# Kernel optimization log

Measured on AMD Instinct MI355X. Metric: run time of the kernel, lower is better.

The kernel has to match this reference:

```python
import jax, jax.numpy as jnp
import numpy as np

N, E, D, H, C, L = 50000, 600000, 128, 128, 40, 2
NEG_SLOPE = 0.1


def setup_inputs() -> dict:
    key = jax.random.key(0)
    ks = jax.random.split(key, 12)

    def lin(k, din, dout):
        return (jax.random.normal(k, (din, dout), jnp.float32) / np.sqrt(din)).astype(jnp.float32)

    x = jax.random.normal(ks[0], (N, D), jnp.float32)
    edge_index = jax.random.randint(ks[1], (2, E), 0, N, dtype=jnp.int32)
    return {
        "x": x,
        "edge_index": edge_index,
        "enc_Wl": lin(ks[2], D, H),
        "enc_Wr": lin(ks[3], D, H),
        "enc_b": jnp.zeros((H,), jnp.float32),
        "lay_Wl": jnp.stack([lin(jax.random.fold_in(ks[4], i), H, H) for i in range(L)]),
        "lay_Wr": jnp.stack([lin(jax.random.fold_in(ks[5], i), H, H) for i in range(L)]),
        "lay_b": jnp.zeros((L, H), jnp.float32),
        "dec_Wl": lin(ks[6], H, C),
        "dec_Wr": lin(ks[7], H, C),
        "dec_b": jnp.zeros((C,), jnp.float32),
    }


def _sage(x, src, dst, inv_cnt, Wl, Wr, b):
    # mean-aggregate neighbor messages: gather x[src], scatter-sum to dst, divide by degree
    agg = jax.ops.segment_sum(x[src], dst, num_segments=N) * inv_cnt  # [N, d_in]
    return agg @ Wl + x @ Wr + b


def reference(x, edge_index, enc_Wl, enc_Wr, enc_b, lay_Wl, lay_Wr, lay_b, dec_Wl, dec_Wr, dec_b):
    src, dst = edge_index[0], edge_index[1]
    # in-degree per target node, clamped to 1 (PyG scatter-mean semantics: isolated nodes get 0)
    deg = jax.ops.segment_sum(jnp.ones((E,), jnp.float32), dst, num_segments=N)
    inv_cnt = (1.0 / jnp.maximum(deg, 1.0))[:, None]  # [N, 1]

    h = jax.nn.leaky_relu(_sage(x, src, dst, inv_cnt, enc_Wl, enc_Wr, enc_b), NEG_SLOPE)
    for i in range(L):
        h = jax.nn.leaky_relu(_sage(h, src, dst, inv_cnt, lay_Wl[i], lay_Wr[i], lay_b[i]), NEG_SLOPE)
    out = _sage(h, src, dst, inv_cnt, dec_Wl, dec_Wr, dec_b)
    return jax.nn.log_softmax(out, axis=1)
```

## Files before the change

kernel.cpp:

```cpp
#include <hip/hip_runtime.h>
#include <hip/hip_bf16.h>

#define NN 50000
#define EE 600000
#define HH 128
#define CC 40
#define NEG 0.1f
#define SCAN_NB 196

typedef __attribute__((ext_vector_type(8))) short bf16x8;
typedef __attribute__((ext_vector_type(4))) float f32x4;

__device__ __forceinline__ unsigned short f2bf(float f) {
    unsigned u = __float_as_uint(f);
    unsigned r = u + 0x7fffu + ((u >> 16) & 1u);
    return (unsigned short)(r >> 16);
}
__device__ __forceinline__ float bfhi(unsigned v) { return __uint_as_float(v & 0xFFFF0000u); }
__device__ __forceinline__ float bflo(unsigned v) { return __uint_as_float(v << 16); }


__global__ void k_count(const int* __restrict__ dst, int* __restrict__ counts) {
    int t = blockIdx.x * blockDim.x + threadIdx.x;
    if (t < EE / 4) {
        int4 d = ((const int4*)dst)[t];
        if ((unsigned)d.x < (unsigned)NN) atomicAdd(&counts[d.x], 1);
        if ((unsigned)d.y < (unsigned)NN) atomicAdd(&counts[d.y], 1);
        if ((unsigned)d.z < (unsigned)NN) atomicAdd(&counts[d.z], 1);
        if ((unsigned)d.w < (unsigned)NN) atomicAdd(&counts[d.w], 1);
    }
}

__global__ void k_scanA(const int* __restrict__ counts, int* __restrict__ blocksums) {
    int t = threadIdx.x, b = blockIdx.x;
    int i = b * 256 + t;
    int v = (i < NN) ? counts[i] : 0;
    for (int off = 1; off < 64; off <<= 1) v += __shfl_xor(v, off, 64);
    __shared__ int ws[4];
    if ((t & 63) == 0) ws[t >> 6] = v;
    __syncthreads();
    if (t == 0) blocksums[b] = ws[0] + ws[1] + ws[2] + ws[3];
}

__global__ void k_scanC(const int* __restrict__ counts, const int* __restrict__ blocksums,
                        int* __restrict__ offsets, int* __restrict__ cursor,
                        float* __restrict__ inv) {
    int t = threadIdx.x, b = blockIdx.x, lane = t & 63, w = t >> 6;
    __shared__ int ws1[4];
    __shared__ int ws2[4];
    int r = (t < SCAN_NB && t < b) ? blocksums[t] : 0;
    for (int off = 1; off < 64; off <<= 1) r += __shfl_xor(r, off, 64);
    if (lane == 0) ws1[w] = r;
    __syncthreads();
    int blockoff = ws1[0] + ws1[1] + ws1[2] + ws1[3];
    int i = b * 256 + t;
    int c = (i < NN) ? counts[i] : 0;
    int v = c;
    for (int off = 1; off < 64; off <<= 1) {
        int u = __shfl_up(v, off, 64);
        if (lane >= off) v += u;
    }
    if (lane == 63) ws2[w] = v;
    __syncthreads();
    int woff = 0;
    for (int j = 0; j < w; ++j) woff += ws2[j];
    int excl = blockoff + woff + (v - c);
    if (i < NN) {
        offsets[i] = excl;
        cursor[i]  = excl;
        inv[i] = (c > 0) ? 1.0f / (float)c : 1.0f;
    }
    if (b == SCAN_NB - 1 && t == 0) offsets[NN] = blockoff + blocksums[SCAN_NB - 1];
}

__global__ void k_scatter(const int* __restrict__ src, const int* __restrict__ dst,
                          int* __restrict__ cursor, int* __restrict__ csr) {
    int t = blockIdx.x * blockDim.x + threadIdx.x;
    if (t < EE / 4) {
        int4 s = ((const int4*)src)[t];
        int4 d = ((const int4*)dst)[t];
        if ((unsigned)d.x < (unsigned)NN) csr[atomicAdd(&cursor[d.x], 1)] = s.x;
        if ((unsigned)d.y < (unsigned)NN) csr[atomicAdd(&cursor[d.y], 1)] = s.y;
        if ((unsigned)d.z < (unsigned)NN) csr[atomicAdd(&cursor[d.z], 1)] = s.z;
        if ((unsigned)d.w < (unsigned)NN) csr[atomicAdd(&cursor[d.w], 1)] = s.w;
    }
}

struct SwzArgs {
    const float* src[8];
    unsigned short* dst[8];
};

template <int DOUT, int DOUTP>
__device__ __forceinline__ void swz_one(const float* __restrict__ W,
                                        unsigned short* __restrict__ dstf, int idx) {
    int k = idx / DOUTP, n = idx % DOUTP;
    unsigned short val = (n < DOUT) ? f2bf(W[k * DOUT + n]) : (unsigned short)0;
    int kt = k >> 5, kin = k & 31, nt = n >> 4, nin = n & 15;
    int lane = ((kin >> 3) << 4) | nin;
    int j = kin & 7;
    int NT = DOUTP >> 4;
    dstf[(((kt * NT + nt) * 64) + lane) * 8 + j] = val;
}

__global__ void k_swz_all(SwzArgs a) {
    int b = blockIdx.x;
    if (b < 384) {
        int which = b >> 6;
        int idx = (b & 63) * 256 + threadIdx.x;
        swz_one<HH, HH>(a.src[which], a.dst[which], idx);
    } else {
        int bb = b - 384;
        int which = 6 + bb / 24;
        int idx = (bb % 24) * 256 + threadIdx.x;
        swz_one<CC, 48>(a.src[which], a.dst[which], idx);
    }
}

template <int NT, int MODE, int INF32>
__global__ __launch_bounds__(256) void k_fused(
    const void* __restrict__ hin_v,
    const int* __restrict__ offsets, const int* __restrict__ csr,
    const float* __restrict__ inv,
    const unsigned short* __restrict__ B1f, const unsigned short* __restrict__ B2f,
    const float* __restrict__ bias, void* __restrict__ out_v) {
    __shared__ unsigned lds[16][72];
    int wid = threadIdx.x >> 6;
    int lane = threadIdx.x & 63;
    int m0 = blockIdx.x * 16;

#pragma unroll
    for (int r = 0; r < 4; ++r) {
        int node = m0 + wid * 4 + r;
        int beg = offsets[node], end = offsets[node + 1];
        float a0 = 0.f, a1 = 0.f;
        int e = beg;
        if (INF32) {
            const float* hf = (const float*)hin_v;
            for (; e + 3 < end; e += 4) {
                int s0 = csr[e], s1 = csr[e + 1], s2 = csr[e + 2], s3 = csr[e + 3];
                float2 v0 = *(const float2*)(hf + s0 * HH + 2 * lane);
                float2 v1 = *(const float2*)(hf + s1 * HH + 2 * lane);
                float2 v2 = *(const float2*)(hf + s2 * HH + 2 * lane);
                float2 v3 = *(const float2*)(hf + s3 * HH + 2 * lane);
                a0 += (v0.x + v1.x) + (v2.x + v3.x);
                a1 += (v0.y + v1.y) + (v2.y + v3.y);
            }
            for (; e < end; ++e) {
                float2 v = *(const float2*)(hf + csr[e] * HH + 2 * lane);
                a0 += v.x; a1 += v.y;
            }
        } else {
            const unsigned* hw = (const unsigned*)hin_v;
            for (; e + 3 < end; e += 4) {
                int s0 = csr[e], s1 = csr[e + 1], s2 = csr[e + 2], s3 = csr[e + 3];
                unsigned v0 = hw[s0 * 64 + lane];
                unsigned v1 = hw[s1 * 64 + lane];
                unsigned v2 = hw[s2 * 64 + lane];
                unsigned v3 = hw[s3 * 64 + lane];
                a0 += (bflo(v0) + bflo(v1)) + (bflo(v2) + bflo(v3));
                a1 += (bfhi(v0) + bfhi(v1)) + (bfhi(v2) + bfhi(v3));
            }
            for (; e < end; ++e) {
                unsigned v = hw[csr[e] * 64 + lane];
                a0 += bflo(v); a1 += bfhi(v);
            }
        }
        float sc = inv[node];
        lds[wid * 4 + r][lane] = ((unsigned)f2bf(a1 * sc) << 16) | (unsigned)f2bf(a0 * sc);
    }
    __syncthreads();

    if (MODE == 1 && wid != 0) return;

    int nin = lane & 15;
    int kq = lane >> 4;
    const unsigned* arow = &lds[nin][0];
    constexpr int TW = (MODE == 0) ? 2 : NT;

    f32x4 acc[TW];
#pragma unroll
    for (int j = 0; j < TW; ++j) acc[j] = (f32x4){0.f, 0.f, 0.f, 0.f};

#pragma unroll
    for (int kt = 0; kt < 4; ++kt) {
        bf16x8 a1 = *(const bf16x8*)(arow + kt * 16 + kq * 4);
        bf16x8 a2;
        if (INF32) {
            const float* hf = (const float*)hin_v;
            const float* rp = hf + (m0 + nin) * HH + kt * 32 + kq * 8;
            float4 p0 = *(const float4*)(rp);
            float4 p1 = *(const float4*)(rp + 4);
            a2[0] = (short)f2bf(p0.x); a2[1] = (short)f2bf(p0.y);
            a2[2] = (short)f2bf(p0.z); a2[3] = (short)f2bf(p0.w);
            a2[4] = (short)f2bf(p1.x); a2[5] = (short)f2bf(p1.y);
            a2[6] = (short)f2bf(p1.z); a2[7] = (short)f2bf(p1.w);
        } else {
            const unsigned short* hb = (const unsigned short*)hin_v;
            a2 = *(const bf16x8*)(hb + (m0 + nin) * HH + kt * 32 + kq * 8);
        }
#pragma unroll
        for (int j = 0; j < TW; ++j) {
            int tile = (MODE == 0) ? (wid * 2 + j) : j;
            bf16x8 b1 = *(const bf16x8*)(B1f + (((kt * NT + tile) * 64) + lane) * 8);
            acc[j] = __builtin_amdgcn_mfma_f32_16x16x32_bf16(a1, b1, acc[j], 0, 0, 0);
        }
#pragma unroll
        for (int j = 0; j < TW; ++j) {
            int tile = (MODE == 0) ? (wid * 2 + j) : j;
            bf16x8 b2 = *(const bf16x8*)(B2f + (((kt * NT + tile) * 64) + lane) * 8);
            acc[j] = __builtin_amdgcn_mfma_f32_16x16x32_bf16(a2, b2, acc[j], 0, 0, 0);
        }
    }

    if (MODE == 0) {
        unsigned short* out = (unsigned short*)out_v;
#pragma unroll
        for (int j = 0; j < TW; ++j) {
            int col = (wid * 2 + j) * 16 + nin;
            float bv = bias[col];
#pragma unroll
            for (int r = 0; r < 4; ++r) {
                int m = m0 + kq * 4 + r;
                float v = acc[j][r] + bv;
                v = fmaxf(v, NEG * v);
                out[m * HH + col] = f2bf(v);
            }
        }
    } else {
        float* out = (float*)out_v;
        float bv[NT];
#pragma unroll
        for (int t = 0; t < NT; ++t) {
            int col = t * 16 + nin;
            bv[t] = (col < CC) ? bias[col] : 0.f;
        }
#pragma unroll
        for (int r = 0; r < 4; ++r) {
            int m = m0 + kq * 4 + r;
            float v[NT];
            float mx = -1e30f;
#pragma unroll
            for (int t = 0; t < NT; ++t) {
                int col = t * 16 + nin;
                v[t] = acc[t][r] + bv[t];
                if (col < CC) mx = fmaxf(mx, v[t]);
            }
            for (int off = 1; off < 16; off <<= 1) mx = fmaxf(mx, __shfl_xor(mx, off, 64));
            float sm = 0.f;
#pragma unroll
            for (int t = 0; t < NT; ++t) {
                int col = t * 16 + nin;
                if (col < CC) sm += expf(v[t] - mx);
            }
            for (int off = 1; off < 16; off <<= 1) sm += __shfl_xor(sm, off, 64);
            float lse = mx + logf(sm);
#pragma unroll
            for (int t = 0; t < NT; ++t) {
                int col = t * 16 + nin;
                if (col < CC) out[m * CC + col] = v[t] - lse;
            }
        }
    }
}

extern "C" void kernel_launch(void* const* d_in, const int* in_sizes, int n_in,
                              void* d_out, int out_size, void* d_ws, size_t ws_size,
                              hipStream_t stream) {
    const float* x      = (const float*)d_in[0];
    const int*   ei     = (const int*)d_in[1];
    const float* enc_Wl = (const float*)d_in[2];
    const float* enc_Wr = (const float*)d_in[3];
    const float* enc_b  = (const float*)d_in[4];
    const float* lay_Wl = (const float*)d_in[5];
    const float* lay_Wr = (const float*)d_in[6];
    const float* lay_b  = (const float*)d_in[7];
    const float* dec_Wl = (const float*)d_in[8];
    const float* dec_Wr = (const float*)d_in[9];
    const float* dec_b  = (const float*)d_in[10];
    float* out = (float*)d_out;

    const int* src = ei;
    const int* dst = ei + EE;

    char* p = (char*)d_ws;
    auto carve = [&](size_t bytes) {
        char* r = p;
        p += (bytes + 255) & ~(size_t)255;
        return r;
    };
    int*            counts    = (int*)carve(NN * 4);
    int*            offsets   = (int*)carve((NN + 1) * 4);
    int*            cursor    = (int*)carve(NN * 4);
    int*            csr       = (int*)carve(EE * 4);
    float*          inv       = (float*)carve(NN * 4);
    int*            blocksums = (int*)carve(SCAN_NB * 4);
    unsigned short* h1        = (unsigned short*)carve((size_t)NN * HH * 2);
    unsigned short* h2        = (unsigned short*)carve((size_t)NN * HH * 2);
    unsigned short* wf[8];
    for (int i = 0; i < 6; ++i) wf[i] = (unsigned short*)carve(HH * HH * 2);
    wf[6] = (unsigned short*)carve(HH * 48 * 2);
    wf[7] = (unsigned short*)carve(HH * 48 * 2);

    {
        SwzArgs a;
        a.src[0] = enc_Wl; a.src[1] = enc_Wr;
        a.src[2] = lay_Wl; a.src[3] = lay_Wr;
        a.src[4] = lay_Wl + HH * HH; a.src[5] = lay_Wr + HH * HH;
        a.src[6] = dec_Wl; a.src[7] = dec_Wr;
        for (int i = 0; i < 8; ++i) a.dst[i] = wf[i];
        k_swz_all<<<432, 256, 0, stream>>>(a);
    }

    hipMemsetAsync(counts, 0, NN * 4, stream);
    int eblk4 = (EE / 4 + 255) / 256;
    k_count<<<eblk4, 256, 0, stream>>>(dst, counts);
    k_scanA<<<SCAN_NB, 256, 0, stream>>>(counts, blocksums);
    k_scanC<<<SCAN_NB, 256, 0, stream>>>(counts, blocksums, offsets, cursor, inv);
    k_scatter<<<eblk4, 256, 0, stream>>>(src, dst, cursor, csr);

    const int FB = NN / 16;
    k_fused<8, 0, 1><<<FB, 256, 0, stream>>>(x,  offsets, csr, inv, wf[0], wf[1], enc_b,      h1);
    k_fused<8, 0, 0><<<FB, 256, 0, stream>>>(h1, offsets, csr, inv, wf[2], wf[3], lay_b,      h2);
    k_fused<8, 0, 0><<<FB, 256, 0, stream>>>(h2, offsets, csr, inv, wf[4], wf[5], lay_b + HH, h1);
    k_fused<3, 1, 0><<<FB, 256, 0, stream>>>(h1, offsets, csr, inv, wf[6], wf[7], dec_b,      out);
}
```

Measured before the change: 348.3 us.

## Gather multiple neighbor rows per wave with wide loads and software prefetch

Reworks the neighbor aggregation so each wave handles its four nodes at once. Lanes are split into groups that each load a full feature row with 16-byte vector loads, so several edges are in flight per wave per round. The next round's loads are issued before the current round is accumulated, and partial sums are then combined across lane groups with cross-lane shuffles. The aim is more memory-level parallelism on the latency-bound gather, at the cost of higher register use, shuffle reductions, and wasted lanes when degrees are uneven.

```diff
diff --git a/kernel.cpp b/kernel.cpp
--- a/kernel.cpp
+++ b/kernel.cpp
@@ -129,45 +129,134 @@
     int lane = threadIdx.x & 63;
     int m0 = blockIdx.x * 16;
 
-#pragma unroll
-    for (int r = 0; r < 4; ++r) {
-        int node = m0 + wid * 4 + r;
-        int beg = offsets[node], end = offsets[node + 1];
-        float a0 = 0.f, a1 = 0.f;
-        int e = beg;
-        if (INF32) {
-            const float* hf = (const float*)hin_v;
-            for (; e + 3 < end; e += 4) {
-                int s0 = csr[e], s1 = csr[e + 1], s2 = csr[e + 2], s3 = csr[e + 3];
-                float2 v0 = *(const float2*)(hf + s0 * HH + 2 * lane);
-                float2 v1 = *(const float2*)(hf + s1 * HH + 2 * lane);
-                float2 v2 = *(const float2*)(hf + s2 * HH + 2 * lane);
-                float2 v3 = *(const float2*)(hf + s3 * HH + 2 * lane);
-                a0 += (v0.x + v1.x) + (v2.x + v3.x);
-                a1 += (v0.y + v1.y) + (v2.y + v3.y);
-            }
-            for (; e < end; ++e) {
-                float2 v = *(const float2*)(hf + csr[e] * HH + 2 * lane);
-                a0 += v.x; a1 += v.y;
-            }
-        } else {
-            const unsigned* hw = (const unsigned*)hin_v;
-            for (; e + 3 < end; e += 4) {
-                int s0 = csr[e], s1 = csr[e + 1], s2 = csr[e + 2], s3 = csr[e + 3];
-                unsigned v0 = hw[s0 * 64 + lane];
-                unsigned v1 = hw[s1 * 64 + lane];
-                unsigned v2 = hw[s2 * 64 + lane];
-                unsigned v3 = hw[s3 * 64 + lane];
-                a0 += (bflo(v0) + bflo(v1)) + (bflo(v2) + bflo(v3));
-                a1 += (bfhi(v0) + bfhi(v1)) + (bfhi(v2) + bfhi(v3));
-            }
-            for (; e < end; ++e) {
-                unsigned v = hw[csr[e] * 64 + lane];
-                a0 += bflo(v); a1 += bfhi(v);
-            }
-        }
-        float sc = inv[node];
-        lds[wid * 4 + r][lane] = ((unsigned)f2bf(a1 * sc) << 16) | (unsigned)f2bf(a0 * sc);
+    int beg[4], end[4];
+    int maxd = 0;
+#pragma unroll
+    for (int n = 0; n < 4; ++n) {
+        int node = m0 + wid * 4 + n;
+        beg[n] = offsets[node];
+        end[n] = offsets[node + 1];
+        int d = end[n] - beg[n];
+        maxd = maxd > d ? maxd : d;
+    }
+
+    if (INF32) {
+        const float4* hf4 = (const float4*)hin_v;
+        int g = lane & 31, s = lane >> 5;
+        float acc[4][4];
+#pragma unroll
+        for (int n = 0; n < 4; ++n)
+#pragma unroll
+            for (int d = 0; d < 4; ++d) acc[n][d] = 0.f;
+        int rounds = (maxd + 1) >> 1;
+
+        float4 v[4]; int ok[4];
+        auto issue = [&](int r, float4* vv, int* okk) {
+#pragma unroll
+            for (int n = 0; n < 4; ++n) {
+                int idx = beg[n] + r * 2 + s;
+                int o = idx < end[n];
+                int row = csr[o ? idx : 0];
+                vv[n] = hf4[(size_t)row * 32 + g];
+                okk[n] = o;
+            }
+        };
+        if (rounds > 0) {
+            issue(0, v, ok);
+            for (int r = 0; r < rounds; ++r) {
+                float4 vn[4]; int okn[4];
+                bool more = (r + 1 < rounds);
+                if (more) issue(r + 1, vn, okn);
+#pragma unroll
+                for (int n = 0; n < 4; ++n) {
+                    if (ok[n]) {
+                        acc[n][0] += v[n].x; acc[n][1] += v[n].y;
+                        acc[n][2] += v[n].z; acc[n][3] += v[n].w;
+                    }
+                }
+                if (more) {
+#pragma unroll
+                    for (int n = 0; n < 4; ++n) { v[n] = vn[n]; ok[n] = okn[n]; }
+                }
+            }
+        }
+#pragma unroll
+        for (int n = 0; n < 4; ++n) {
+#pragma unroll
+            for (int d = 0; d < 4; ++d) {
+                float t = acc[n][d];
+                t += __shfl_xor(t, 32, 64);
+                acc[n][d] = t;
+            }
+            float sc = inv[m0 + wid * 4 + n];
+            if (s == 0) {
+                unsigned d0 = ((unsigned)f2bf(acc[n][1] * sc) << 16) | f2bf(acc[n][0] * sc);
+                unsigned d1 = ((unsigned)f2bf(acc[n][3] * sc) << 16) | f2bf(acc[n][2] * sc);
+                uint2 w2; w2.x = d0; w2.y = d1;
+                *(uint2*)&lds[wid * 4 + n][2 * g] = w2;
+            }
+        }
+    } else {
+        const uint4* hw4 = (const uint4*)hin_v;
+        int g = lane & 15, s = lane >> 4;
+        float acc[4][8];
+#pragma unroll
+        for (int n = 0; n < 4; ++n)
+#pragma unroll
+            for (int d = 0; d < 8; ++d) acc[n][d] = 0.f;
+        int rounds = (maxd + 3) >> 2;
+
+        uint4 v[4]; int ok[4];
+        auto issue = [&](int r, uint4* vv, int* okk) {
+#pragma unroll
+            for (int n = 0; n < 4; ++n) {
+                int idx = beg[n] + r * 4 + s;
+                int o = idx < end[n];
+                int row = csr[o ? idx : 0];
+                vv[n] = hw4[(size_t)row * 16 + g];
+                okk[n] = o;
+            }
+        };
+        if (rounds > 0) {
+            issue(0, v, ok);
+            for (int r = 0; r < rounds; ++r) {
+                uint4 vn[4]; int okn[4];
+                bool more = (r + 1 < rounds);
+                if (more) issue(r + 1, vn, okn);
+#pragma unroll
+                for (int n = 0; n < 4; ++n) {
+                    if (ok[n]) {
+                        acc[n][0] += bflo(v[n].x); acc[n][1] += bfhi(v[n].x);
+                        acc[n][2] += bflo(v[n].y); acc[n][3] += bfhi(v[n].y);
+                        acc[n][4] += bflo(v[n].z); acc[n][5] += bfhi(v[n].z);
+                        acc[n][6] += bflo(v[n].w); acc[n][7] += bfhi(v[n].w);
+                    }
+                }
+                if (more) {
+#pragma unroll
+                    for (int n = 0; n < 4; ++n) { v[n] = vn[n]; ok[n] = okn[n]; }
+                }
+            }
+        }
+#pragma unroll
+        for (int n = 0; n < 4; ++n) {
+#pragma unroll
+            for (int d = 0; d < 8; ++d) {
+                float t = acc[n][d];
+                t += __shfl_xor(t, 16, 64);
+                t += __shfl_xor(t, 32, 64);
+                acc[n][d] = t;
+            }
+            float sc = inv[m0 + wid * 4 + n];
+            if (s == 0) {
+                uint4 w4;
+                w4.x = ((unsigned)f2bf(acc[n][1] * sc) << 16) | f2bf(acc[n][0] * sc);
+                w4.y = ((unsigned)f2bf(acc[n][3] * sc) << 16) | f2bf(acc[n][2] * sc);
+                w4.z = ((unsigned)f2bf(acc[n][5] * sc) << 16) | f2bf(acc[n][4] * sc);
+                w4.w = ((unsigned)f2bf(acc[n][7] * sc) << 16) | f2bf(acc[n][6] * sc);
+                *(uint4*)&lds[wid * 4 + n][4 * g] = w4;
+            }
+        }
     }
     __syncthreads();
 
```

Result: faster. 339.5 us (-2.5%).
